# Performance work log

Hardware: AMD Instinct MI355X
Metric: run time of the kernel (lower is better)

Reference implementation:

```python
import jax, jax.numpy as jnp
import numpy as np

B, C, IMG, P, D, NH, NL = 64, 3, 224, 16, 768, 12, 12
G = IMG // P
T = G * G  # 196 patches
EPS = 1e-5


def setup_inputs():
    key = jax.random.key(0)
    ks = jax.random.split(key, 8)
    x = jax.random.normal(ks[0], (B, C, IMG, IMG), jnp.float32)
    context_mask = jax.random.uniform(ks[1], (B, T)) < 0.5
    context_mask = context_mask.at[:, 0].set(True)  # guarantee >=1 visible token per sample
    s = 0.02
    patch_w = jax.random.normal(ks[2], (D, C, P, P), jnp.float32) * s
    patch_b = jnp.zeros((D,), jnp.float32)
    pos_embed = jax.random.normal(ks[3], (1, T, D), jnp.float32)
    in_proj_w = jax.random.normal(ks[4], (NL, 3 * D, D), jnp.float32) * s
    in_proj_b = jnp.zeros((NL, 3 * D), jnp.float32)
    out_w = jax.random.normal(ks[5], (NL, D, D), jnp.float32) * s
    out_b = jnp.zeros((NL, D), jnp.float32)
    ffn_w1 = jax.random.normal(ks[6], (NL, 4 * D, D), jnp.float32) * s
    ffn_b1 = jnp.zeros((NL, 4 * D), jnp.float32)
    ffn_w2 = jax.random.normal(ks[7], (NL, D, 4 * D), jnp.float32) * s
    ffn_b2 = jnp.zeros((NL, D), jnp.float32)
    ln1_g = jnp.ones((NL, D), jnp.float32); ln1_b = jnp.zeros((NL, D), jnp.float32)
    ln2_g = jnp.ones((NL, D), jnp.float32); ln2_b = jnp.zeros((NL, D), jnp.float32)
    norm_g = jnp.ones((D,), jnp.float32); norm_b = jnp.zeros((D,), jnp.float32)
    return dict(x=x, context_mask=context_mask, patch_w=patch_w, patch_b=patch_b,
                pos_embed=pos_embed, in_proj_w=in_proj_w, in_proj_b=in_proj_b,
                out_w=out_w, out_b=out_b, ln1_g=ln1_g, ln1_b=ln1_b,
                ffn_w1=ffn_w1, ffn_b1=ffn_b1, ffn_w2=ffn_w2, ffn_b2=ffn_b2,
                ln2_g=ln2_g, ln2_b=ln2_b, norm_g=norm_g, norm_b=norm_b)


def _layer_norm(x, g, b):
    m = jnp.mean(x, -1, keepdims=True)
    v = jnp.mean((x - m) ** 2, -1, keepdims=True)
    return (x - m) * jax.lax.rsqrt(v + EPS) * g + b


def _mha(x, pad, wqkv, bqkv, wo, bo):
    Bq, S, Dm = x.shape
    hd = Dm // NH
    qkv = x @ wqkv.T + bqkv
    q, k, v = jnp.split(qkv, 3, axis=-1)
    sp = lambda t: t.reshape(Bq, S, NH, hd).transpose(0, 2, 1, 3)
    q, k, v = sp(q), sp(k), sp(v)
    scores = jnp.einsum('bhqd,bhkd->bhqk', q, k) / jnp.sqrt(jnp.float32(hd))
    scores = jnp.where(pad[:, None, None, :], jnp.float32(-1e30), scores)  # mask pad keys
    attn = jax.nn.softmax(scores, axis=-1)
    out = jnp.einsum('bhqk,bhkd->bhqd', attn, v).transpose(0, 2, 1, 3).reshape(Bq, S, Dm)
    return out @ wo.T + bo


def _encode(x, context_mask, patch_w, patch_b, pos_embed, in_proj_w, in_proj_b,
            out_w, out_b, ln1_g, ln1_b, ffn_w1, ffn_b1, ffn_w2, ffn_b2,
            ln2_g, ln2_b, norm_g, norm_b, Sc):
    # patch embedding: strided conv == non-overlapping patch projection
    t = jax.lax.conv_general_dilated(x, patch_w, (P, P), 'VALID')  # [B,D,G,G]
    t = t.reshape(x.shape[0], D, T).transpose(0, 2, 1) + patch_b   # [B,T,D]
    t = t + pos_embed  # gather(tokens)+gather(pos) == gather(tokens+pos) for same indices
    lengths = jnp.sum(context_mask, axis=1)                        # [B]
    # stable argsort puts True (visible) indices first, in ascending order == nonzero()
    order = jnp.argsort(~context_mask, axis=1, stable=True)[:, :Sc]
    ctx = jnp.take_along_axis(t, order[:, :, None], axis=1)        # [B,Sc,D]
    ctx_pad = jnp.arange(Sc)[None, :] >= lengths[:, None]          # True = pad
    ctx = jnp.where(ctx_pad[:, :, None], jnp.float32(0.0), ctx)    # zero-fill pads
    for l in range(NL):
        a = _mha(ctx, ctx_pad, in_proj_w[l], in_proj_b[l], out_w[l], out_b[l])
        ctx = _layer_norm(ctx + a, ln1_g[l], ln1_b[l])
        h = jax.nn.gelu(ctx @ ffn_w1[l].T + ffn_b1[l], approximate=False)
        ctx = _layer_norm(ctx + h @ ffn_w2[l].T + ffn_b2[l], ln2_g[l], ln2_b[l])
    ctx = _layer_norm(ctx, norm_g, norm_b)
    return ctx, ctx_pad


def reference(x, context_mask, patch_w, patch_b, pos_embed, in_proj_w, in_proj_b,
              out_w, out_b, ln1_g, ln1_b, ffn_w1, ffn_b1, ffn_w2, ffn_b2,
              ln2_g, ln2_b, norm_g, norm_b):
    # Sc = max context length (data-dependent, computed on host from concrete mask)
    Sc = int(np.max(np.asarray(jnp.sum(context_mask, axis=1))))
    return _encode(x, context_mask, patch_w, patch_b, pos_embed, in_proj_w, in_proj_b,
                   out_w, out_b, ln1_g, ln1_b, ffn_w1, ffn_b1, ffn_w2, ffn_b2,
                   ln2_g, ln2_b, norm_g, norm_b, Sc)
```

## Files before the change

kernel.cpp:

```cpp
#include <hip/hip_runtime.h>
#include <math.h>

#define BB 64
#define IMG 224
#define PP 16
#define DD 768
#define NH 12
#define NL 12
#define GG 14
#define TT 196
#define HD 64

typedef __attribute__((ext_vector_type(8))) short short8;
typedef __attribute__((ext_vector_type(4))) float floatx4;

__device__ __forceinline__ unsigned short f2bfu(float f) {
    union { float f; unsigned int u; } v; v.f = f;
    unsigned int r = v.u + 0x7FFFu + ((v.u >> 16) & 1u);
    return (unsigned short)(r >> 16);
}

__device__ __forceinline__ void g2lds16(const void* g, void* l) {
    __builtin_amdgcn_global_load_lds(
        (const __attribute__((address_space(1))) unsigned int*)g,
        (__attribute__((address_space(3))) unsigned int*)l, 16, 0, 0);
}

template <int MODE>
__global__ __launch_bounds__(256) void gemm_mfma(const unsigned short* __restrict__ A,
                                                 const unsigned short* __restrict__ W,
                                                 const float* __restrict__ bias,
                                                 float* __restrict__ Cf,
                                                 unsigned short* __restrict__ Cb,
                                                 int M, int N, int K,
                                                 const float* __restrict__ pose) {
    __shared__ unsigned short As[128 * 32];
    __shared__ unsigned short Bs[128 * 32];
    const int nb = N >> 7;
    const int m0 = (blockIdx.x / nb) << 7;
    const int n0 = (blockIdx.x % nb) << 7;
    const int tid = threadIdx.x;
    const int lane = tid & 63;
    const int wave = tid >> 6;
    const int wm = (wave >> 1) << 6;
    const int wn = (wave & 1) << 6;
    const int fr = lane & 15;
    const int fk = (lane >> 4) << 3;

    const unsigned short* Ag = A + (size_t)(m0 + (tid >> 2)) * K + (tid & 3) * 8;
    const unsigned short* Wg = W + (size_t)(n0 + (tid >> 2)) * K + (tid & 3) * 8;
    unsigned short* lA = As + tid * 8;
    unsigned short* lB = Bs + tid * 8;
    const size_t rowskip = (size_t)64 * K;

    floatx4 acc[4][4];
#pragma unroll
    for (int i = 0; i < 4; ++i)
#pragma unroll
        for (int j = 0; j < 4; ++j) acc[i][j] = (floatx4){0.f, 0.f, 0.f, 0.f};

    for (int kt = 0; kt < K; kt += 32) {
        g2lds16(Ag + kt, lA);
        g2lds16(Ag + kt + rowskip, lA + 64 * 32);
        g2lds16(Wg + kt, lB);
        g2lds16(Wg + kt + rowskip, lB + 64 * 32);
        __syncthreads();
        short8 af[4], bf[4];
#pragma unroll
        for (int i = 0; i < 4; ++i) {
            af[i] = *(const short8*)(As + (wm + i * 16 + fr) * 32 + fk);
            bf[i] = *(const short8*)(Bs + (wn + i * 16 + fr) * 32 + fk);
        }
#pragma unroll
        for (int i = 0; i < 4; ++i)
#pragma unroll
            for (int j = 0; j < 4; ++j)
                acc[i][j] = __builtin_amdgcn_mfma_f32_16x16x32_bf16(af[i], bf[j], acc[i][j], 0, 0, 0);
        __syncthreads();
    }

    const int r0 = (lane >> 4) << 2;
#pragma unroll
    for (int j = 0; j < 4; ++j) {
        const int col = n0 + wn + j * 16 + fr;
        const float bv = bias[col];
#pragma unroll
        for (int i = 0; i < 4; ++i) {
            const int row = m0 + wm + i * 16 + r0;
#pragma unroll
            for (int r = 0; r < 4; ++r) {
                float v = acc[i][j][r] + bv;
                if (MODE == 1) {
                    v = 0.5f * v * (1.0f + erff(v * 0.70710678118654752f));
                    Cb[(size_t)(row + r) * N + col] = f2bfu(v);
                } else if (MODE == 2) {
                    const int tok = (row + r) % TT;
                    Cf[(size_t)(row + r) * N + col] = v + pose[(size_t)tok * DD + col];
                } else if (MODE == 3) {
                    Cb[(size_t)(row + r) * N + col] = f2bfu(v);
                } else {
                    Cf[(size_t)(row + r) * N + col] = v;
                }
            }
        }
    }
}

__global__ __launch_bounds__(256) void im2col_bf16(const float* __restrict__ x,
                                                   unsigned short* __restrict__ A) {
    const int u = blockIdx.x * 256 + threadIdx.x;
    const int m = u / 192;
    const int kq = (u - m * 192) * 4;
    const int b = m / TT, token = m - b * TT;
    const int gy = token / GG, gx = token - gy * GG;
    const int c = kq >> 8, py = (kq >> 4) & 15, px = kq & 15;
    const float* src = x + ((size_t)b * 3 + c) * (IMG * IMG)
                         + (size_t)(gy * PP + py) * IMG + gx * PP + px;
    float4 v = *(const float4*)src;
    ushort4 o;
    o.x = f2bfu(v.x); o.y = f2bfu(v.y); o.z = f2bfu(v.z); o.w = f2bfu(v.w);
    *(ushort4*)(A + (size_t)m * DD + kq) = o;
}

__global__ __launch_bounds__(256) void patch_embed_gemm(const float* __restrict__ x,
                                                        const float* __restrict__ W,
                                                        const float* __restrict__ bias,
                                                        const float* __restrict__ pos,
                                                        float* __restrict__ t) {
    __shared__ float Asm[16][68];
    __shared__ float Bsm[16][68];
    const int m0 = (blockIdx.x / 12) * 64;
    const int n0 = (blockIdx.x % 12) * 64;
    const int tid = threadIdx.x;
    const int lr = tid >> 2;
    const int lk = (tid & 3) * 4;
    const int tx = tid & 15, ty = tid >> 4;

    const int m = m0 + lr;
    const int b = m / TT, token = m % TT;
    const int gy = token / GG, gx = token % GG;
    const float* xrow = x + (size_t)b * (3 * IMG * IMG) + (gy * PP) * IMG + gx * PP;

    float acc[4][4] = {};
    for (int kt = 0; kt < 48; ++kt) {
        int c = kt >> 4, py = kt & 15;
        float4 av = *(const float4*)(xrow + ((size_t)c * IMG + py) * IMG + lk);
        float4 bv = *(const float4*)(W + (size_t)(n0 + lr) * DD + kt * 16 + lk);
        __syncthreads();
        Asm[lk + 0][lr] = av.x; Asm[lk + 1][lr] = av.y; Asm[lk + 2][lr] = av.z; Asm[lk + 3][lr] = av.w;
        Bsm[lk + 0][lr] = bv.x; Bsm[lk + 1][lr] = bv.y; Bsm[lk + 2][lr] = bv.z; Bsm[lk + 3][lr] = bv.w;
        __syncthreads();
#pragma unroll
        for (int k = 0; k < 16; ++k) {
            float4 a4 = *(const float4*)&Asm[k][ty * 4];
            float4 b4 = *(const float4*)&Bsm[k][tx * 4];
            float a[4] = {a4.x, a4.y, a4.z, a4.w};
            float b2[4] = {b4.x, b4.y, b4.z, b4.w};
#pragma unroll
            for (int i = 0; i < 4; ++i)
#pragma unroll
                for (int j = 0; j < 4; ++j) acc[i][j] += a[i] * b2[j];
        }
    }
    float4 bi = *(const float4*)(bias + n0 + tx * 4);
#pragma unroll
    for (int i = 0; i < 4; ++i) {
        int mi = m0 + ty * 4 + i;
        int tok = mi % TT;
        float4 p4 = *(const float4*)(pos + (size_t)tok * DD + n0 + tx * 4);
        float4 o;
        o.x = acc[i][0] + bi.x + p4.x;
        o.y = acc[i][1] + bi.y + p4.y;
        o.z = acc[i][2] + bi.z + p4.z;
        o.w = acc[i][3] + bi.w + p4.w;
        *(float4*)(t + (size_t)mi * DD + n0 + tx * 4) = o;
    }
}

__global__ __launch_bounds__(64) void scan_mask(const unsigned char* __restrict__ mask8,
                                                int* __restrict__ order,
                                                int* __restrict__ lengths,
                                                float* __restrict__ pad_out, int Sc) {
    const int b = blockIdx.x;
    const int lane = threadIdx.x;
    const unsigned int* w = (const unsigned int*)mask8;
    unsigned int v0 = w[lane];
    unsigned long long bf = __ballot(v0 == 0x3F800000u);
    unsigned long long bg = __ballot(v0 != 0x3F800000u && v0 > 1u);
    const int mode = bf ? 2 : (bg ? 1 : 0);
    int cnt = 0;
    for (int i0 = 0; i0 < TT; i0 += 64) {
        const int i = i0 + lane;
        int mv = 0;
        if (i < TT) {
            if (mode == 0) mv = mask8[4 * (b * TT + i)];
            else if (mode == 1) mv = mask8[b * TT + i];
            else mv = (w[b * TT + i] != 0u);
        }
        unsigned long long bal = __ballot(mv != 0);
        int pre = __popcll(bal & ((1ull << lane) - 1ull));
        if (mv) order[b * Sc + cnt + pre] = i;
        cnt += __popcll(bal);
    }
    if (lane == 0) lengths[b] = cnt;
    for (int s = lane; s < Sc; s += 64) pad_out[b * Sc + s] = (s < cnt) ? 0.f : 1.f;
}

__global__ __launch_bounds__(256) void gather_copy(const float* __restrict__ t,
                                                   const int* __restrict__ order,
                                                   const int* __restrict__ lengths,
                                                   float* __restrict__ ctx,
                                                   unsigned short* __restrict__ ctxb, int Sc) {
    const int total = BB * Sc * (DD / 4);
    for (int u = blockIdx.x * 256 + threadIdx.x; u < total; u += gridDim.x * 256) {
        const int row = u / 192, q = u - row * 192;
        const int b = row / Sc, s = row - b * Sc;
        float4 v = {0.f, 0.f, 0.f, 0.f};
        if (s < lengths[b])
            v = *(const float4*)(t + ((size_t)b * TT + order[b * Sc + s]) * DD + q * 4);
        *(float4*)(ctx + (size_t)row * DD + q * 4) = v;
        ushort4 o;
        o.x = f2bfu(v.x); o.y = f2bfu(v.y); o.z = f2bfu(v.z); o.w = f2bfu(v.w);
        *(ushort4*)(ctxb + (size_t)row * DD + q * 4) = o;
    }
}

template <int P>
__global__ __launch_bounds__(256) void attn_mfma(const unsigned short* __restrict__ qkv,
                                                 const int* __restrict__ lengths,
                                                 unsigned short* __restrict__ outp, int Sc) {
    constexpr int PS = 64 * P;
    constexpr int KROW = 128;
    constexpr int VROW = PS * 2;
    extern __shared__ unsigned char smraw[];
    unsigned char* Kb = smraw;
    unsigned char* Vt = Kb + PS * KROW;
    unsigned char* Pw = Vt + 64 * VROW;
    const int b = blockIdx.x / NH, h = blockIdx.x % NH;
    const int len = lengths[b];
    const int tid = threadIdx.x;
    const int lane = tid & 63, wave = tid >> 6;
    const int fr = lane & 15, g = lane >> 4;
    const size_t qbase = (size_t)b * Sc * (3 * DD) + h * HD;

    for (int c = tid; c < PS * 8; c += 256) {
        const int s = c >> 3, kg = c & 7;
        short8 kv = {0, 0, 0, 0, 0, 0, 0, 0};
        short8 vv = {0, 0, 0, 0, 0, 0, 0, 0};
        if (s < len) {
            kv = *(const short8*)(qkv + qbase + (size_t)s * (3 * DD) + DD + kg * 8);
            vv = *(const short8*)(qkv + qbase + (size_t)s * (3 * DD) + 2 * DD + kg * 8);
        }
        *(short8*)(Kb + s * KROW + ((kg * 16) ^ ((s & 7) << 4))) = kv;
#pragma unroll
        for (int e = 0; e < 8; ++e) {
            const int d = kg * 8 + e;
            *(unsigned short*)(Vt + d * VROW + ((s * 2) ^ ((d & 7) << 4))) =
                (unsigned short)vv[e];
        }
    }
    __syncthreads();

    const int wq0 = wave * 16 * P;
    short8 qf[P][2];
#pragma unroll
    for (int i = 0; i < P; ++i) {
        int qr = wq0 + i * 16 + fr; if (qr >= Sc) qr = Sc - 1;
#pragma unroll
        for (int ks = 0; ks < 2; ++ks)
            qf[i][ks] = *(const short8*)(qkv + qbase + (size_t)qr * (3 * DD) + ks * 32 + g * 8);
    }

    floatx4 sacc[P][4 * P];
#pragma unroll
    for (int i = 0; i < P; ++i)
#pragma unroll
        for (int j = 0; j < 4 * P; ++j) sacc[i][j] = (floatx4){0.f, 0.f, 0.f, 0.f};
#pragma unroll
    for (int j = 0; j < 4 * P; ++j) {
        const int key = j * 16 + fr;
#pragma unroll
        for (int ks = 0; ks < 2; ++ks) {
            short8 kf = *(const short8*)(Kb + key * KROW + ((ks * 64 + g * 16) ^ ((key & 7) << 4)));
#pragma unroll
            for (int i = 0; i < P; ++i)
                sacc[i][j] = __builtin_amdgcn_mfma_f32_16x16x32_bf16(qf[i][ks], kf, sacc[i][j], 0, 0, 0);
        }
    }

    unsigned char* mypw = Pw + (size_t)wave * (16 * P) * VROW;
#pragma unroll
    for (int i = 0; i < P; ++i) {
#pragma unroll
        for (int r = 0; r < 4; ++r) {
            float vals[4 * P];
            float vmax = -1e30f;
#pragma unroll
            for (int j = 0; j < 4 * P; ++j) {
                float s = sacc[i][j][r] * 0.125f;
                if (j * 16 + fr >= len) s = -1e30f;
                vals[j] = s;
                vmax = fmaxf(vmax, s);
            }
#pragma unroll
            for (int off = 1; off < 16; off <<= 1) vmax = fmaxf(vmax, __shfl_xor(vmax, off, 64));
            float lsum = 0.f;
#pragma unroll
            for (int j = 0; j < 4 * P; ++j) { vals[j] = __expf(vals[j] - vmax); lsum += vals[j]; }
#pragma unroll
            for (int off = 1; off < 16; off <<= 1) lsum += __shfl_xor(lsum, off, 64);
            const float rl = 1.0f / lsum;
            const int lr = i * 16 + g * 4 + r;
            unsigned char* rowp = mypw + lr * VROW;
            const int sw = (lr & 7) << 4;
#pragma unroll
            for (int j = 0; j < 4 * P; ++j)
                *(unsigned short*)(rowp + (((j * 16 + fr) * 2) ^ sw)) = f2bfu(vals[j] * rl);
        }
    }

    floatx4 oacc[P][4];
#pragma unroll
    for (int i = 0; i < P; ++i)
#pragma unroll
        for (int dt = 0; dt < 4; ++dt) oacc[i][dt] = (floatx4){0.f, 0.f, 0.f, 0.f};
#pragma unroll
    for (int kk = 0; kk < 2 * P; ++kk) {
        short8 pa[P];
#pragma unroll
        for (int i = 0; i < P; ++i) {
            const int lr = i * 16 + fr;
            pa[i] = *(const short8*)(mypw + lr * VROW + ((kk * 64 + g * 16) ^ ((lr & 7) << 4)));
        }
#pragma unroll
        for (int dt = 0; dt < 4; ++dt) {
            const int d = dt * 16 + fr;
            short8 vb = *(const short8*)(Vt + d * VROW + ((kk * 64 + g * 16) ^ ((d & 7) << 4)));
#pragma unroll
            for (int i = 0; i < P; ++i)
                oacc[i][dt] = __builtin_amdgcn_mfma_f32_16x16x32_bf16(pa[i], vb, oacc[i][dt], 0, 0, 0);
        }
    }

#pragma unroll
    for (int i = 0; i < P; ++i) {
#pragma unroll
        for (int r = 0; r < 4; ++r) {
            const int qr = wq0 + i * 16 + g * 4 + r;
            if (qr < Sc) {
#pragma unroll
                for (int dt = 0; dt < 4; ++dt)
                    outp[((size_t)b * Sc + qr) * DD + h * HD + dt * 16 + fr] = f2bfu(oacc[i][dt][r]);
            }
        }
    }
}

template <int P>
__global__ __launch_bounds__(512) void attn_v3(const float* __restrict__ qkv,
                                               const int* __restrict__ lengths,
                                               unsigned short* __restrict__ outp, int Sc) {
    extern __shared__ float smem[];
    float* pst = smem;
    float* qst = pst + 8 * P * 64;
    float* Ks  = qst + 8 * 66;
    float* Vs  = Ks + P * 64 * 66;
    const int b = blockIdx.x / NH, h = blockIdx.x % NH;
    const int len = lengths[b];
    const int tid = threadIdx.x;
    const float* base = qkv + (size_t)b * Sc * (3 * DD) + h * HD;

    for (int idx = tid; idx < Sc * HD; idx += 512) {
        int s = idx >> 6, d = idx & 63;
        Ks[s * 66 + d] = base[(size_t)s * (3 * DD) + DD + d];
        Vs[s * 66 + d] = base[(size_t)s * (3 * DD) + 2 * DD + d];
    }
    __syncthreads();

    const int wave = tid >> 6, lane = tid & 63;
    float* qw = qst + wave * 66;
    float* pw = pst + wave * P * 64;

    for (int q = wave; q < Sc; q += 8) {
        float qv = base[(size_t)q * (3 * DD) + lane];
        qw[lane] = qv;
        float s0 = 0.f, s1 = 0.f, s2 = 0.f, s3 = 0.f;
#pragma unroll
        for (int d0 = 0; d0 < 64; d0 += 2) {
            float2 q2 = *(const float2*)(qw + d0);
            float2 k0 = *(const float2*)(Ks + lane * 66 + d0);
            s0 += q2.x * k0.x + q2.y * k0.y;
            if (P > 1) {
                float2 k1 = *(const float2*)(Ks + (lane + 64) * 66 + d0);
                s1 += q2.x * k1.x + q2.y * k1.y;
            }
            if (P > 2) {
                float2 k2 = *(const float2*)(Ks + (lane + 128) * 66 + d0);
                s2 += q2.x * k2.x + q2.y * k2.y;
            }
            if (P > 3) {
                float2 k3 = *(const float2*)(Ks + (lane + 192) * 66 + d0);
                s3 += q2.x * k3.x + q2.y * k3.y;
            }
        }
        s0 = (lane < len) ? s0 * 0.125f : -1e30f;
        if (P > 1) s1 = (64 + lane < len) ? s1 * 0.125f : -1e30f;
        if (P > 2) s2 = (128 + lane < len) ? s2 * 0.125f : -1e30f;
        if (P > 3) s3 = (192 + lane < len) ? s3 * 0.125f : -1e30f;
        float m = s0;
        if (P > 1) m = fmaxf(m, s1);
        if (P > 2) m = fmaxf(m, s2);
        if (P > 3) m = fmaxf(m, s3);
#pragma unroll
        for (int off = 32; off; off >>= 1) m = fmaxf(m, __shfl_xor(m, off, 64));
        s0 = __expf(s0 - m);
        if (P > 1) s1 = __expf(s1 - m);
        if (P > 2) s2 = __expf(s2 - m);
        if (P > 3) s3 = __expf(s3 - m);
        float l = s0;
        if (P > 1) l += s1;
        if (P > 2) l += s2;
        if (P > 3) l += s3;
#pragma unroll
        for (int off = 32; off; off >>= 1) l += __shfl_xor(l, off, 64);
        pw[lane] = s0;
        if (P > 1) pw[64 + lane] = s1;
        if (P > 2) pw[128 + lane] = s2;
        if (P > 3) pw[192 + lane] = s3;
        float a0 = 0.f, a1 = 0.f, a2 = 0.f, a3 = 0.f;
        const int j4 = len & ~3;
        for (int j = 0; j < j4; j += 4) {
            float4 p4 = *(const float4*)(pw + j);
            a0 += p4.x * Vs[(j + 0) * 66 + lane];
            a1 += p4.y * Vs[(j + 1) * 66 + lane];
            a2 += p4.z * Vs[(j + 2) * 66 + lane];
            a3 += p4.w * Vs[(j + 3) * 66 + lane];
        }
        for (int j = j4; j < len; ++j) a0 += pw[j] * Vs[j * 66 + lane];
        float acc = (a0 + a1) + (a2 + a3);
        outp[((size_t)b * Sc + q) * DD + h * HD + lane] = f2bfu(acc / l);
    }
}

__global__ __launch_bounds__(256) void ln_kernel(const float* __restrict__ x,
                                                 const float* __restrict__ yadd,
                                                 const float* __restrict__ g,
                                                 const float* __restrict__ beta,
                                                 float* __restrict__ outf,
                                                 unsigned short* __restrict__ outb) {
    __shared__ float red[4];
    const size_t row = blockIdx.x;
    const int tid = threadIdx.x;
    float v[3];
#pragma unroll
    for (int i = 0; i < 3; ++i) {
        int d = tid + i * 256;
        float t0 = x[row * DD + d];
        if (yadd) t0 += yadd[row * DD + d];
        v[i] = t0;
    }
    float s = v[0] + v[1] + v[2];
#pragma unroll
    for (int off = 32; off; off >>= 1) s += __shfl_xor(s, off, 64);
    if ((tid & 63) == 0) red[tid >> 6] = s;
    __syncthreads();
    float mean = (red[0] + red[1] + red[2] + red[3]) * (1.0f / 768.0f);
    __syncthreads();
    float vs = 0.f;
#pragma unroll
    for (int i = 0; i < 3; ++i) { float d0 = v[i] - mean; vs += d0 * d0; }
#pragma unroll
    for (int off = 32; off; off >>= 1) vs += __shfl_xor(vs, off, 64);
    if ((tid & 63) == 0) red[tid >> 6] = vs;
    __syncthreads();
    float var = (red[0] + red[1] + red[2] + red[3]) * (1.0f / 768.0f);
    float inv = rsqrtf(var + 1e-5f);
#pragma unroll
    for (int i = 0; i < 3; ++i) {
        int d = tid + i * 256;
        float o = (v[i] - mean) * inv * g[d] + beta[d];
        outf[row * DD + d] = o;
        if (outb) outb[row * DD + d] = f2bfu(o);
    }
}

__global__ __launch_bounds__(256) void convert4_bf16(const float* __restrict__ a, int na,
                                                     const float* __restrict__ b, int nb,
                                                     const float* __restrict__ c, int nc,
                                                     const float* __restrict__ d, int nd,
                                                     unsigned short* __restrict__ dst) {
    const int total4 = (na + nb + nc + nd) >> 2;
    for (int u = blockIdx.x * 256 + threadIdx.x; u < total4; u += gridDim.x * 256) {
        int e = u << 2;
        const float* src; int off;
        if (e < na) { src = a; off = e; }
        else if (e < na + nb) { src = b; off = e - na; }
        else if (e < na + nb + nc) { src = c; off = e - na - nb; }
        else { src = d; off = e - na - nb - nc; }
        float4 v = *(const float4*)(src + off);
        ushort4 o;
        o.x = f2bfu(v.x); o.y = f2bfu(v.y); o.z = f2bfu(v.z); o.w = f2bfu(v.w);
        *(ushort4*)(dst + e) = o;
    }
}

extern "C" void kernel_launch(void* const* d_in, const int* in_sizes, int n_in,
                              void* d_out, int out_size, void* d_ws, size_t ws_size,
                              hipStream_t stream) {
    (void)in_sizes; (void)n_in; (void)ws_size;
    const float* x          = (const float*)d_in[0];
    const unsigned char* mk = (const unsigned char*)d_in[1];
    const float* patch_w    = (const float*)d_in[2];
    const float* patch_b    = (const float*)d_in[3];
    const float* pos        = (const float*)d_in[4];
    const float* in_proj_w  = (const float*)d_in[5];
    const float* in_proj_b  = (const float*)d_in[6];
    const float* out_w      = (const float*)d_in[7];
    const float* out_b      = (const float*)d_in[8];
    const float* ln1_g      = (const float*)d_in[9];
    const float* ln1_b      = (const float*)d_in[10];
    const float* ffn_w1     = (const float*)d_in[11];
    const float* ffn_b1     = (const float*)d_in[12];
    const float* ffn_w2     = (const float*)d_in[13];
    const float* ffn_b2     = (const float*)d_in[14];
    const float* ln2_g      = (const float*)d_in[15];
    const float* ln2_b      = (const float*)d_in[16];
    const float* norm_g     = (const float*)d_in[17];
    const float* norm_b     = (const float*)d_in[18];
    float* out = (float*)d_out;

    const int Sc = out_size / (BB * (DD + 1));
    const int M = BB * Sc;
    const int Mp = ((M + 127) / 128) * 128;
    const int MB = Mp / 128;

    float* t_f   = (float*)d_ws;
    float* qkv_f = t_f + (size_t)BB * TT * DD;
    float* ctx_f = qkv_f + (size_t)Mp * 2304;
    float* y_f   = ctx_f + (size_t)Mp * DD;
    unsigned short* ctx_b  = (unsigned short*)(y_f + (size_t)Mp * DD);
    unsigned short* attn_b = ctx_b + (size_t)Mp * DD;
    unsigned short* h_b    = attn_b + (size_t)Mp * DD;
    unsigned short* wq     = h_b + (size_t)Mp * 4 * DD;
    unsigned short* wo     = wq + (size_t)3 * DD * DD;
    unsigned short* w1     = wo + (size_t)DD * DD;
    unsigned short* w2     = w1 + (size_t)4 * DD * DD;
    int* lengths = (int*)(w2 + (size_t)4 * DD * DD);
    unsigned short* qkv_b = (unsigned short*)qkv_f;
    int* order = (int*)qkv_f;

    const bool fast_patch =
        ((size_t)Mp * 2304 * sizeof(float) >= (size_t)BB * TT * DD * sizeof(unsigned short)) &&
        ((size_t)Mp * DD * sizeof(unsigned short) >= (size_t)DD * DD * sizeof(unsigned short));
    if (fast_patch) {
        unsigned short* Apatch = ((unsigned short*)qkv_f) + (size_t)BB * 256;
        unsigned short* wpatch = ctx_b;
        im2col_bf16<<<(BB * TT * DD / 4) / 256, 256, 0, stream>>>(x, Apatch);
        convert4_bf16<<<1024, 256, 0, stream>>>(patch_w, DD * DD, nullptr, 0,
                                                nullptr, 0, nullptr, 0, wpatch);
        gemm_mfma<2><<<(BB * TT / 128) * (DD / 128), 256, 0, stream>>>(
            Apatch, wpatch, patch_b, t_f, nullptr, BB * TT, DD, DD, pos);
        order = (int*)(Apatch + (size_t)BB * TT * DD);
    } else {
        patch_embed_gemm<<<TT * 12, 256, 0, stream>>>(x, patch_w, patch_b, pos, t_f);
    }
    scan_mask<<<BB, 64, 0, stream>>>(mk, order, lengths, out + (size_t)M * DD, Sc);
    {
        int total4 = BB * Sc * (DD / 4);
        int gblocks = (total4 + 255) / 256; if (gblocks > 2048) gblocks = 2048;
        gather_copy<<<gblocks, 256, 0, stream>>>(t_f, order, lengths, ctx_f, ctx_b, Sc);
    }

    int P = (Sc + 63) / 64; if (P > 4) P = 4;
    const bool mfma_attn = (P <= 2);
    size_t smem_attn;
    if (mfma_attn) {
        smem_attn = (size_t)(64 * P) * 128 * (2 + P);
        const void* fp = (P == 1) ? (const void*)attn_mfma<1> : (const void*)attn_mfma<2>;
        (void)hipFuncSetAttribute(fp, hipFuncAttributeMaxDynamicSharedMemorySize, (int)smem_attn);
    } else {
        smem_attn = (size_t)(8 * P * 64 + 8 * 66 + (size_t)(P * 64 + Sc) * 66) * sizeof(float);
        const void* fp = (P == 3) ? (const void*)attn_v3<3> : (const void*)attn_v3<4>;
        (void)hipFuncSetAttribute(fp, hipFuncAttributeMaxDynamicSharedMemorySize, (int)smem_attn);
    }

    for (int l = 0; l < NL; ++l) {
        convert4_bf16<<<1024, 256, 0, stream>>>(
            in_proj_w + (size_t)l * 3 * DD * DD, 3 * DD * DD,
            out_w + (size_t)l * DD * DD, DD * DD,
            ffn_w1 + (size_t)l * 4 * DD * DD, 4 * DD * DD,
            ffn_w2 + (size_t)l * 4 * DD * DD, 4 * DD * DD, wq);
        if (mfma_attn) {
            gemm_mfma<3><<<MB * 18, 256, 0, stream>>>(ctx_b, wq, in_proj_b + (size_t)l * 3 * DD,
                                                      nullptr, qkv_b, Mp, 3 * DD, DD, nullptr);
            if (P == 1)
                attn_mfma<1><<<BB * NH, 256, smem_attn, stream>>>(qkv_b, lengths, attn_b, Sc);
            else
                attn_mfma<2><<<BB * NH, 256, smem_attn, stream>>>(qkv_b, lengths, attn_b, Sc);
        } else {
            gemm_mfma<0><<<MB * 18, 256, 0, stream>>>(ctx_b, wq, in_proj_b + (size_t)l * 3 * DD,
                                                      qkv_f, nullptr, Mp, 3 * DD, DD, nullptr);
            if (P == 3)
                attn_v3<3><<<BB * NH, 512, smem_attn, stream>>>(qkv_f, lengths, attn_b, Sc);
            else
                attn_v3<4><<<BB * NH, 512, smem_attn, stream>>>(qkv_f, lengths, attn_b, Sc);
        }
        gemm_mfma<0><<<MB * 6, 256, 0, stream>>>(attn_b, wo, out_b + (size_t)l * DD,
                                                 y_f, nullptr, Mp, DD, DD, nullptr);
        ln_kernel<<<M, 256, 0, stream>>>(ctx_f, y_f, ln1_g + (size_t)l * DD,
                                         ln1_b + (size_t)l * DD, ctx_f, ctx_b);
        gemm_mfma<1><<<MB * 24, 256, 0, stream>>>(ctx_b, w1, ffn_b1 + (size_t)l * 4 * DD,
                                                  nullptr, h_b, Mp, 4 * DD, DD, nullptr);
        gemm_mfma<0><<<MB * 6, 256, 0, stream>>>(h_b, w2, ffn_b2 + (size_t)l * DD,
                                                 y_f, nullptr, Mp, DD, 4 * DD, nullptr);
        ln_kernel<<<M, 256, 0, stream>>>(ctx_f, y_f, ln2_g + (size_t)l * DD,
                                         ln2_b + (size_t)l * DD, ctx_f, ctx_b);
    }
    ln_kernel<<<M, 256, 0, stream>>>(ctx_f, nullptr, norm_g, norm_b, out, nullptr);
}
```

Baseline: 3.716 ms.

## Split-K the out-projection and FFN2 GEMMs, reducing partial sums inside LayerNorm

Adds a split-K mode to the MFMA GEMM. The out-projection is split into 2 K-chunks and FFN down-projection into 3 K-chunks, and each writes fp32 partial results into the now-free QKV scratch buffer. The LayerNorm kernel sums the partials together with the residual, so no extra reduction kernel is needed. The N=768 GEMMs only produce a few hundred tiles, which underfills the GPU; splitting K multiplies the block count. The cost is extra fp32 partial writes and reads.

Measured after the change: 3.762 ms. Within noise of the previous version (+1.3%).

```diff
diff --git a/kernel.cpp b/kernel.cpp
--- a/kernel.cpp
+++ b/kernel.cpp
@@ -33,12 +33,20 @@
                                                  float* __restrict__ Cf,
                                                  unsigned short* __restrict__ Cb,
                                                  int M, int N, int K,
-                                                 const float* __restrict__ pose) {
+                                                 const float* __restrict__ pose,
+                                                 int klen, int splits) {
     __shared__ unsigned short As[128 * 32];
     __shared__ unsigned short Bs[128 * 32];
     const int nb = N >> 7;
-    const int m0 = (blockIdx.x / nb) << 7;
-    const int n0 = (blockIdx.x % nb) << 7;
+    int bid = blockIdx.x;
+    int split = 0;
+    if (MODE == 4) {
+        const int per = gridDim.x / splits;
+        split = bid / per;
+        bid -= split * per;
+    }
+    const int m0 = (bid / nb) << 7;
+    const int n0 = (bid % nb) << 7;
     const int tid = threadIdx.x;
     const int lane = tid & 63;
     const int wave = tid >> 6;
@@ -59,7 +67,9 @@
 #pragma unroll
         for (int j = 0; j < 4; ++j) acc[i][j] = (floatx4){0.f, 0.f, 0.f, 0.f};
 
-    for (int kt = 0; kt < K; kt += 32) {
+    const int kstart = (MODE == 4) ? split * klen : 0;
+    const int kend = (MODE == 4) ? kstart + klen : K;
+    for (int kt = kstart; kt < kend; kt += 32) {
         g2lds16(Ag + kt, lA);
         g2lds16(Ag + kt + rowskip, lA + 64 * 32);
         g2lds16(Wg + kt, lB);
@@ -79,11 +89,13 @@
         __syncthreads();
     }
 
+    float* Cfs = (MODE == 4) ? Cf + (size_t)split * M * N : Cf;
     const int r0 = (lane >> 4) << 2;
 #pragma unroll
     for (int j = 0; j < 4; ++j) {
         const int col = n0 + wn + j * 16 + fr;
-        const float bv = bias[col];
+        float bv = bias ? bias[col] : 0.f;
+        if (MODE == 4 && split != 0) bv = 0.f;
 #pragma unroll
         for (int i = 0; i < 4; ++i) {
             const int row = m0 + wm + i * 16 + r0;
@@ -95,11 +107,11 @@
                     Cb[(size_t)(row + r) * N + col] = f2bfu(v);
                 } else if (MODE == 2) {
                     const int tok = (row + r) % TT;
-                    Cf[(size_t)(row + r) * N + col] = v + pose[(size_t)tok * DD + col];
+                    Cfs[(size_t)(row + r) * N + col] = v + pose[(size_t)tok * DD + col];
                 } else if (MODE == 3) {
                     Cb[(size_t)(row + r) * N + col] = f2bfu(v);
                 } else {
-                    Cf[(size_t)(row + r) * N + col] = v;
+                    Cfs[(size_t)(row + r) * N + col] = v;
                 }
             }
         }
@@ -443,7 +455,8 @@
 }
 
 __global__ __launch_bounds__(256) void ln_kernel(const float* __restrict__ x,
-                                                 const float* __restrict__ yadd,
+                                                 const float* __restrict__ parts,
+                                                 int nparts, size_t pstride,
                                                  const float* __restrict__ g,
                                                  const float* __restrict__ beta,
                                                  float* __restrict__ outf,
@@ -456,7 +469,7 @@
     for (int i = 0; i < 3; ++i) {
         int d = tid + i * 256;
         float t0 = x[row * DD + d];
-        if (yadd) t0 += yadd[row * DD + d];
+        for (int s = 0; s < nparts; ++s) t0 += parts[s * pstride + row * DD + d];
         v[i] = t0;
     }
     float s = v[0] + v[1] + v[2];
@@ -548,6 +561,7 @@
     int* lengths = (int*)(w2 + (size_t)4 * DD * DD);
     unsigned short* qkv_b = (unsigned short*)qkv_f;
     int* order = (int*)qkv_f;
+    const size_t pstr = (size_t)Mp * DD;
 
     const bool fast_patch =
         ((size_t)Mp * 2304 * sizeof(float) >= (size_t)BB * TT * DD * sizeof(unsigned short)) &&
@@ -559,7 +573,7 @@
         convert4_bf16<<<1024, 256, 0, stream>>>(patch_w, DD * DD, nullptr, 0,
                                                 nullptr, 0, nullptr, 0, wpatch);
         gemm_mfma<2><<<(BB * TT / 128) * (DD / 128), 256, 0, stream>>>(
-            Apatch, wpatch, patch_b, t_f, nullptr, BB * TT, DD, DD, pos);
+            Apatch, wpatch, patch_b, t_f, nullptr, BB * TT, DD, DD, pos, DD, 1);
         order = (int*)(Apatch + (size_t)BB * TT * DD);
     } else {
         patch_embed_gemm<<<TT * 12, 256, 0, stream>>>(x, patch_w, patch_b, pos, t_f);
@@ -592,29 +606,29 @@
             ffn_w2 + (size_t)l * 4 * DD * DD, 4 * DD * DD, wq);
         if (mfma_attn) {
             gemm_mfma<3><<<MB * 18, 256, 0, stream>>>(ctx_b, wq, in_proj_b + (size_t)l * 3 * DD,
-                                                      nullptr, qkv_b, Mp, 3 * DD, DD, nullptr);
+                                                      nullptr, qkv_b, Mp, 3 * DD, DD, nullptr, DD, 1);
             if (P == 1)
                 attn_mfma<1><<<BB * NH, 256, smem_attn, stream>>>(qkv_b, lengths, attn_b, Sc);
             else
                 attn_mfma<2><<<BB * NH, 256, smem_attn, stream>>>(qkv_b, lengths, attn_b, Sc);
         } else {
             gemm_mfma<0><<<MB * 18, 256, 0, stream>>>(ctx_b, wq, in_proj_b + (size_t)l * 3 * DD,
-                                                      qkv_f, nullptr, Mp, 3 * DD, DD, nullptr);
+                                                      qkv_f, nullptr, Mp, 3 * DD, DD, nullptr, DD, 1);
             if (P == 3)
                 attn_v3<3><<<BB * NH, 512, smem_attn, stream>>>(qkv_f, lengths, attn_b, Sc);
             else
                 attn_v3<4><<<BB * NH, 512, smem_attn, stream>>>(qkv_f, lengths, attn_b, Sc);
         }
-        gemm_mfma<0><<<MB * 6, 256, 0, stream>>>(attn_b, wo, out_b + (size_t)l * DD,
-                                                 y_f, nullptr, Mp, DD, DD, nullptr);
-        ln_kernel<<<M, 256, 0, stream>>>(ctx_f, y_f, ln1_g + (size_t)l * DD,
+        gemm_mfma<4><<<2 * MB * 6, 256, 0, stream>>>(attn_b, wo, out_b + (size_t)l * DD,
+                                                     qkv_f, nullptr, Mp, DD, DD, nullptr, 384, 2);
+        ln_kernel<<<M, 256, 0, stream>>>(ctx_f, qkv_f, 2, pstr, ln1_g + (size_t)l * DD,
                                          ln1_b + (size_t)l * DD, ctx_f, ctx_b);
         gemm_mfma<1><<<MB * 24, 256, 0, stream>>>(ctx_b, w1, ffn_b1 + (size_t)l * 4 * DD,
-                                                  nullptr, h_b, Mp, 4 * DD, DD, nullptr);
-        gemm_mfma<0><<<MB * 6, 256, 0, stream>>>(h_b, w2, ffn_b2 + (size_t)l * DD,
-                                                 y_f, nullptr, Mp, DD, 4 * DD, nullptr);
-        ln_kernel<<<M, 256, 0, stream>>>(ctx_f, y_f, ln2_g + (size_t)l * DD,
+                                                  nullptr, h_b, Mp, 4 * DD, DD, nullptr, DD, 1);
+        gemm_mfma<4><<<3 * MB * 6, 256, 0, stream>>>(h_b, w2, ffn_b2 + (size_t)l * DD,
+                                                     qkv_f, nullptr, Mp, DD, 4 * DD, nullptr, 1024, 3);
+        ln_kernel<<<M, 256, 0, stream>>>(ctx_f, qkv_f, 3, pstr, ln2_g + (size_t)l * DD,
                                          ln2_b + (size_t)l * DD, ctx_f, ctx_b);
     }
-    ln_kernel<<<M, 256, 0, stream>>>(ctx_f, nullptr, norm_g, norm_b, out, nullptr);
-}
+    ln_kernel<<<M, 256, 0, stream>>>(ctx_f, nullptr, 0, 0, norm_g, norm_b, out, nullptr);
+}
```
